# Kernel tuning notes

Hardware: AMD Instinct MI355X
Metric: run time of the kernel (lower is better)

## Reference

```python
import jax, jax.numpy as jnp
import numpy as np

N_HEADS = 1
D_MODEL = 128
TOP_K = 64
BATCH = 4
SEQ = 4096


def _rope_tables(T, d_head):
    # div_term = 10000**(arange(0,d,2)/d), repeat_interleave(2); even slice recovers the base freqs
    pos = jnp.arange(T, dtype=jnp.float32)[:, None]            # (T,1)
    div = 10000.0 ** (jnp.arange(0, d_head, 2, dtype=jnp.float32) / d_head)  # (d/2,)
    ang = pos / div[None, :]                                    # (T, d/2)
    return jnp.cos(ang), jnp.sin(ang)


def _apply_rope(x, cos, sin):
    # x: (..., T, d); cos/sin: (T, d/2) broadcast over leading dims
    xe = x[..., 0::2]
    xo = x[..., 1::2]
    re = xe * cos - xo * sin
    ro = xe * sin + xo * cos
    return jnp.stack([re, ro], axis=-1).reshape(x.shape)


def setup_inputs() -> dict:
    key = jax.random.key(0)
    kq, kk, kv = jax.random.split(key, 3)
    q = jax.random.normal(kq, (BATCH, SEQ, D_MODEL), dtype=jnp.float32)
    k = jax.random.normal(kk, (BATCH, SEQ, D_MODEL), dtype=jnp.float32)
    v = jax.random.normal(kv, (BATCH, SEQ, D_MODEL), dtype=jnp.float32)
    return {"q": q, "k": k, "v": v}


def reference(q, k, v):
    b, T, d_model = q.shape
    H = N_HEADS
    D = d_model // H  # d_head; module only valid for H=1 (k is never head-split)
    qh = q.reshape(b, T, H, D).transpose(0, 2, 1, 3)   # (b,H,T,D)
    vh = v.reshape(b, T, H, D).transpose(0, 2, 1, 3)   # (b,H,T,D)
    kh = k[:, None, :, :]                              # (b,1,T,d_model) == (b,H,T,D) for H=1

    cos, sin = _rope_tables(T, D)
    qh = _apply_rope(qh, cos, sin)
    kh = _apply_rope(kh, cos, sin)

    scale = 1.0 / jnp.sqrt(jnp.asarray(D, dtype=qh.dtype))
    logits = jnp.einsum('bhtd,bhsd->bhts', qh, kh) * scale   # (b,H,T,T)

    idx = jnp.arange(T)
    causal = idx[None, :] <= idx[:, None]                    # (T,T): key j <= query i
    logits = jnp.where(causal[None, None], logits, -jnp.inf)

    topk_vals, topk_idx = jax.lax.top_k(logits, TOP_K)       # (b,H,T,K)
    attn = jax.nn.softmax(topk_vals, axis=-1)                # -inf rows -> 0 weight

    bi = jnp.arange(b)[:, None, None, None]
    hi = jnp.arange(H)[None, :, None, None]
    topk_v = vh[bi, hi, topk_idx]                            # (b,H,T,K,D)
    out = jnp.einsum('bhtk,bhtkd->bhtd', attn, topk_v)       # (b,H,T,D)
    return out.transpose(0, 2, 1, 3).reshape(b, T, d_model)
```

## Files before the change

kernel.cpp:

```cpp
#include <hip/hip_runtime.h>
#include <math.h>

#define BATCH 4
#define SEQ   4096
#define DM    128
#define TOPK  64
#define SCALE 0.08838834764831845f
#define CAP   384

typedef short bf16x8 __attribute__((ext_vector_type(8)));
typedef float f32x4  __attribute__((ext_vector_type(4)));

__device__ __forceinline__ unsigned short f2bf(float x) {
    unsigned u = __float_as_uint(x);
    u += 0x7FFFu + ((u >> 16) & 1u);
    return (unsigned short)(u >> 16);
}
__device__ __forceinline__ float bf2f(unsigned short h) {
    return __uint_as_float(((unsigned)h) << 16);
}
__device__ __forceinline__ void split3(float x, unsigned short& h,
                                       unsigned short& md, unsigned short& l) {
    h = f2bf(x);
    float r1 = x - bf2f(h);
    md = f2bf(r1);
    float r2 = r1 - bf2f(md);
    l = f2bf(r2);
}

__device__ __forceinline__ unsigned fmap(float f) {
    unsigned u = __float_as_uint(f);
    return (u & 0x80000000u) ? ~u : (u | 0x80000000u);
}
__device__ __forceinline__ float finv(unsigned u) {
    return (u & 0x80000000u) ? __uint_as_float(u & 0x7FFFFFFFu) : __uint_as_float(~u);
}
__device__ __forceinline__ float wave_fmax(float v) {
    #pragma unroll
    for (int m = 32; m; m >>= 1) v = fmaxf(v, __shfl_xor(v, m));
    return v;
}
__device__ __forceinline__ float wave_fsum(float v) {
    #pragma unroll
    for (int m = 32; m; m >>= 1) v += __shfl_xor(v, m);
    return v;
}
__device__ __forceinline__ unsigned wave_umax(unsigned v) {
    #pragma unroll
    for (int m = 32; m; m >>= 1) { unsigned o = __shfl_xor(v, m); v = (o > v) ? o : v; }
    return v;
}

__device__ __forceinline__ float ztail(float p) {
    float pp = (p <= 0.5f) ? p : (1.f - p);
    float tt = sqrtf(-2.f * logf(pp));
    float z = tt - (2.30753f + 0.27061f * tt) / (1.f + 0.99229f * tt + 0.04481f * tt * tt);
    return (p <= 0.5f) ? z : -z;
}

__global__ void rope_decomp(const float* __restrict__ q, const float* __restrict__ k,
                            unsigned short* __restrict__ qh, unsigned short* __restrict__ qm,
                            unsigned short* __restrict__ ql, unsigned short* __restrict__ kh,
                            unsigned short* __restrict__ km, unsigned short* __restrict__ kl) {
    int idx = blockIdx.x * blockDim.x + threadIdx.x;
    const int total = BATCH * SEQ * (DM / 2);
    if (idx >= total) return;
    int i   = idx & 63;
    int pos = (idx >> 6) & (SEQ - 1);
    int b   = idx >> 18;
    float dv  = powf(10000.0f, (float)(2 * i) / (float)DM);
    float ang = (float)pos / dv;
    float sn, cs;
    sincosf(ang, &sn, &cs);
    size_t base = ((size_t)b * SEQ + pos) * DM + 2 * i;
    float qe = q[base], qo = q[base + 1];
    float ke = k[base], ko = k[base + 1];
    float q0 = (qe * cs - qo * sn) * SCALE, q1 = (qe * sn + qo * cs) * SCALE;
    float k0 = ke * cs - ko * sn,          k1 = ke * sn + ko * cs;
    unsigned short h, m2, l;
    split3(q0, h, m2, l); qh[base] = h;     qm[base] = m2;     ql[base] = l;
    split3(q1, h, m2, l); qh[base + 1] = h; qm[base + 1] = m2; ql[base + 1] = l;
    split3(k0, h, m2, l); kh[base] = h;     km[base] = m2;     kl[base] = l;
    split3(k1, h, m2, l); kh[base + 1] = h; km[base + 1] = m2; kl[base + 1] = l;
}

__launch_bounds__(256, 2)
__global__ void logits_mfma(const unsigned short* __restrict__ qh, const unsigned short* __restrict__ qm,
                            const unsigned short* __restrict__ ql, const unsigned short* __restrict__ kh,
                            const unsigned short* __restrict__ km, const unsigned short* __restrict__ kl,
                            float* __restrict__ lg, int r0, int m, int stride) {
    const int st = blockIdx.x, qt = blockIdx.y, b = blockIdx.z;
    const int Q0 = r0 + qt * 128, S0 = st * 128;
    if (S0 > Q0 + 127) return;
    const int tid = threadIdx.x, lane = tid & 63, w = tid >> 6;
    const int wm = (w >> 1) * 64, wn = (w & 1) * 64;
    if (S0 + wn > Q0 + wm + 63) return;

    const int rA = Q0 + wm + (lane & 15);
    const int rB = S0 + wn + (lane & 15);
    const int dc = (lane >> 4) * 8;

    f32x4 acc[4][4] = {};
    #pragma unroll
    for (int kk = 0; kk < 4; ++kk) {
        const int doff = kk * 32 + dc;
        bf16x8 Ah[4], Am[4], Al[4], Bh[4], Bm[4], Bl[4];
        #pragma unroll
        for (int i = 0; i < 4; ++i) {
            size_t qoff = ((size_t)b * SEQ + rA + i * 16) * DM + doff;
            Ah[i] = *(const bf16x8*)(qh + qoff);
            Am[i] = *(const bf16x8*)(qm + qoff);
            Al[i] = *(const bf16x8*)(ql + qoff);
            size_t koff = ((size_t)b * SEQ + rB + i * 16) * DM + doff;
            Bh[i] = *(const bf16x8*)(kh + koff);
            Bm[i] = *(const bf16x8*)(km + koff);
            Bl[i] = *(const bf16x8*)(kl + koff);
        }
        #pragma unroll
        for (int i = 0; i < 4; ++i)
            #pragma unroll
            for (int j = 0; j < 4; ++j) {
                f32x4 c = acc[i][j];
                c = __builtin_amdgcn_mfma_f32_16x16x32_bf16(Ah[i], Bh[j], c, 0, 0, 0);
                c = __builtin_amdgcn_mfma_f32_16x16x32_bf16(Ah[i], Bm[j], c, 0, 0, 0);
                c = __builtin_amdgcn_mfma_f32_16x16x32_bf16(Am[i], Bh[j], c, 0, 0, 0);
                c = __builtin_amdgcn_mfma_f32_16x16x32_bf16(Ah[i], Bl[j], c, 0, 0, 0);
                c = __builtin_amdgcn_mfma_f32_16x16x32_bf16(Al[i], Bh[j], c, 0, 0, 0);
                c = __builtin_amdgcn_mfma_f32_16x16x32_bf16(Am[i], Bm[j], c, 0, 0, 0);
                acc[i][j] = c;
            }
    }

    const int colb = lane & 15, rowb = (lane >> 4) * 4;
    #pragma unroll
    for (int i = 0; i < 4; ++i) {
        #pragma unroll
        for (int r = 0; r < 4; ++r) {
            int qrow = Q0 + wm + i * 16 + rowb + r;
            size_t base = ((size_t)(b * m + (qrow - r0))) * stride;
            #pragma unroll
            for (int j = 0; j < 4; ++j) {
                int col = S0 + wn + j * 16 + colb;
                if (col <= qrow) lg[base + col] = acc[i][j][r];
            }
        }
    }
}

__launch_bounds__(256)
__global__ void select_out2(const float* __restrict__ lg, const float* __restrict__ v,
                            float* __restrict__ out, int r0, int m, int stride) {
    __shared__ unsigned long long bufK[4][CAP];
    __shared__ float sW[4][TOPK];
    __shared__ int   sI[4][TOPK];

    const int w = threadIdx.x >> 6, lane = threadIdx.x & 63;
    const int x = blockIdx.x * 4 + w, b = blockIdx.y;
    if (x >= m) return;
    const int t = r0 + x, n = t + 1;
    const float* row = lg + ((size_t)(b * m + x)) * stride;
    const float4* row4 = (const float4*)row;
    const int nv4 = n >> 2, rem = n & 3;
    const unsigned long long lmask = (1ull << lane) - 1ull;

    if (n <= TOPK) {
        float val = (lane < n) ? row[lane] : -3.0e38f;
        float M = wave_fmax(val);
        float wgt = (lane < n) ? expf(val - M) : 0.f;
        float S = wave_fsum(wgt);
        sW[w][lane] = wgt;
        float inv = 1.f / S;
        float a0 = 0.f, a1 = 0.f;
        for (int j = 0; j < n; ++j) {
            float wj = sW[w][j];
            size_t base = ((size_t)b * SEQ + j) * DM;
            a0 += wj * v[base + lane];
            a1 += wj * v[base + 64 + lane];
        }
        size_t ob = ((size_t)b * SEQ + t) * DM;
        out[ob + lane] = a0 * inv;
        out[ob + 64 + lane] = a1 * inv;
        return;
    }

    float T, zt = 0.f;
    if (n <= CAP - 32) T = -3.0e38f;
    else { zt = ztail(128.f / (float)n); T = zt; }

    float Tlo = -3.3e38f, Thi = 3.3e38f;
    int C = 0;
    unsigned um = 0u;
    for (int it = 0; it < 12; ++it) {
        C = 0;
        unsigned lm = 0u;
        for (int i0 = 0; i0 < nv4; i0 += 64) {
            const int i = i0 + lane;
            const bool inb = (i < nv4);
            float4 r4;
            if (inb) r4 = row4[i];
            else { r4.x = -3.4e38f; r4.y = -3.4e38f; r4.z = -3.4e38f; r4.w = -3.4e38f; }
            const int s = i << 2;
            bool p0 = inb && (r4.x >= T);
            unsigned long long m0 = __ballot(p0);
            if (p0) { unsigned u = fmap(r4.x); lm = u > lm ? u : lm; int pos = C + __popcll(m0 & lmask); if (pos < CAP) bufK[w][pos] = ((unsigned long long)u << 32) | (unsigned)(SEQ - s); }
            C += (int)__popcll(m0);
            bool p1 = inb && (r4.y >= T);
            unsigned long long m1 = __ballot(p1);
            if (p1) { unsigned u = fmap(r4.y); lm = u > lm ? u : lm; int pos = C + __popcll(m1 & lmask); if (pos < CAP) bufK[w][pos] = ((unsigned long long)u << 32) | (unsigned)(SEQ - (s + 1)); }
            C += (int)__popcll(m1);
            bool p2 = inb && (r4.z >= T);
            unsigned long long m2 = __ballot(p2);
            if (p2) { unsigned u = fmap(r4.z); lm = u > lm ? u : lm; int pos = C + __popcll(m2 & lmask); if (pos < CAP) bufK[w][pos] = ((unsigned long long)u << 32) | (unsigned)(SEQ - (s + 2)); }
            C += (int)__popcll(m2);
            bool p3 = inb && (r4.w >= T);
            unsigned long long m3 = __ballot(p3);
            if (p3) { unsigned u = fmap(r4.w); lm = u > lm ? u : lm; int pos = C + __popcll(m3 & lmask); if (pos < CAP) bufK[w][pos] = ((unsigned long long)u << 32) | (unsigned)(SEQ - (s + 3)); }
            C += (int)__popcll(m3);
        }
        {
            float val = -3.4e38f;
            if (lane < rem) val = row[nv4 * 4 + lane];
            bool pt = (lane < rem) && (val >= T);
            unsigned long long mt = __ballot(pt);
            if (pt) { unsigned u = fmap(val); lm = u > lm ? u : lm; int pos = C + __popcll(mt & lmask); if (pos < CAP) bufK[w][pos] = ((unsigned long long)u << 32) | (unsigned)(SEQ - (nv4 * 4 + lane)); }
            C += (int)__popcll(mt);
        }
        um = wave_umax(lm);
        if (C >= TOPK && C <= CAP) break;
        if (C < TOPK) Thi = fminf(Thi, T); else Tlo = fmaxf(Tlo, T);
        float Tn; bool okc = false;
        float phat = (float)(C < 1 ? 1 : C) / (float)n;
        if (phat < 0.45f && T > 0.05f) {
            float zh = ztail(phat);
            if (zh > 0.05f) { Tn = T * (zt / zh); okc = true; }
        }
        if (!okc || !(Tn > Tlo && Tn < Thi)) {
            if (Tlo > -3.2e38f && Thi < 3.2e38f) Tn = 0.5f * (Tlo + Thi);
            else if (C < TOPK)                   Tn = T - 0.5f;
            else                                 Tn = T + 0.4f;
        }
        T = Tn;
    }
    const float M = finv(um);
    int Cw = C; if (Cw > CAP) Cw = CAP;

    sW[w][lane] = 0.f; sI[w][lane] = 0;

    for (int c0 = lane; c0 < Cw; c0 += 64) {
        unsigned long long kc = bufK[w][c0];
        int r = 0;
        for (int j = 0; j < Cw; ++j) r += (bufK[w][j] > kc);
        if (r < TOPK) {
            sW[w][r] = expf(finv((unsigned)(kc >> 32)) - M);
            sI[w][r] = SEQ - (int)(kc & 0xFFFFFFFFu);
        }
    }
    float S = wave_fsum(sW[w][lane]);
    float inv = 1.f / S;

    const int sub = lane & 31, halfw = lane >> 5;
    f32x4 a4 = {0.f, 0.f, 0.f, 0.f};
    for (int j2 = halfw; j2 < TOPK; j2 += 2) {
        float wj = sW[w][j2];
        const float4* vr = (const float4*)(v + ((size_t)b * SEQ + sI[w][j2]) * DM) + sub;
        float4 vv = *vr;
        a4.x += wj * vv.x; a4.y += wj * vv.y; a4.z += wj * vv.z; a4.w += wj * vv.w;
    }
    a4.x += __shfl_xor(a4.x, 32);
    a4.y += __shfl_xor(a4.y, 32);
    a4.z += __shfl_xor(a4.z, 32);
    a4.w += __shfl_xor(a4.w, 32);
    if (halfw == 0) {
        float4 o4;
        o4.x = a4.x * inv; o4.y = a4.y * inv; o4.z = a4.z * inv; o4.w = a4.w * inv;
        *((float4*)(out + ((size_t)b * SEQ + t) * DM) + sub) = o4;
    }
}

__global__ void rope_prep(const float* __restrict__ q, const float* __restrict__ k,
                          float* __restrict__ rq, float* __restrict__ rk) {
    int idx = blockIdx.x * blockDim.x + threadIdx.x;
    const int total = BATCH * SEQ * (DM / 2);
    if (idx >= total) return;
    int i   = idx & 63;
    int pos = (idx >> 6) & (SEQ - 1);
    int b   = idx >> 18;
    float dv  = powf(10000.0f, (float)(2 * i) / (float)DM);
    float ang = (float)pos / dv;
    float sn, cs;
    sincosf(ang, &sn, &cs);
    size_t base = ((size_t)b * SEQ + pos) * DM + 2 * i;
    float qe = q[base], qo = q[base + 1];
    float ke = k[base], ko = k[base + 1];
    rq[base]     = qe * cs - qo * sn;
    rq[base + 1] = qe * sn + qo * cs;
    rk[base]     = ke * cs - ko * sn;
    rk[base + 1] = ke * sn + ko * cs;
}

__launch_bounds__(256)
__global__ void topk_attn(const float* __restrict__ rq, const float* __restrict__ rk,
                          const float* __restrict__ v, float* __restrict__ out) {
    __shared__ unsigned umap[SEQ];
    __shared__ float    qs[DM];
    __shared__ int      selIdx[TOPK];
    __shared__ float    selW[TOPK];
    __shared__ int      cnt;
    __shared__ float    redf[4];
    __shared__ int      redi[4];
    __shared__ float    sMax, sSum;

    const int t   = blockIdx.x & (SEQ - 1);
    const int b   = blockIdx.x >> 12;
    const int tid = threadIdx.x;
    const int lane = tid & 63, wid = tid >> 6;
    const int n = t + 1;

    if (tid < DM) qs[tid] = rq[((size_t)b * SEQ + t) * DM + tid];
    if (tid == 0) cnt = 0;
    __syncthreads();

    float lmax = -INFINITY;
    for (int s = tid; s < n; s += 256) {
        const float4* kr = (const float4*)(rk + ((size_t)b * SEQ + s) * DM);
        const float4* qr = (const float4*)qs;
        float acc = 0.f;
        #pragma unroll
        for (int d = 0; d < DM / 4; ++d) {
            float4 kv = kr[d]; float4 qv = qr[d];
            acc += kv.x * qv.x + kv.y * qv.y + kv.z * qv.z + kv.w * qv.w;
        }
        float lgv = acc * SCALE;
        umap[s] = fmap(lgv);
        lmax = fmaxf(lmax, lgv);
    }
    #pragma unroll
    for (int off = 32; off; off >>= 1) lmax = fmaxf(lmax, __shfl_down(lmax, off));
    if (lane == 0) redf[wid] = lmax;
    __syncthreads();
    if (tid == 0) sMax = fmaxf(fmaxf(redf[0], redf[1]), fmaxf(redf[2], redf[3]));
    __syncthreads();
    const float M = sMax;

    const int K = (n < TOPK) ? n : TOPK;
    unsigned thr = 0u;
    if (n > TOPK) {
        unsigned long long lo = 0ull, hi = (unsigned long long)fmap(M);
        while (lo < hi) {
            unsigned long long mid = (lo + hi + 1ull) >> 1;
            unsigned m32 = (unsigned)mid;
            int c = 0;
            for (int s = tid; s < n; s += 256) c += (umap[s] >= m32) ? 1 : 0;
            #pragma unroll
            for (int off = 32; off; off >>= 1) c += __shfl_down(c, off);
            if (lane == 0) redi[wid] = c;
            __syncthreads();
            int tot = redi[0] + redi[1] + redi[2] + redi[3];
            __syncthreads();
            if (tot >= K) lo = mid; else hi = mid - 1ull;
        }
        thr = (unsigned)lo;
    }

    for (int s = tid; s < n; s += 256) {
        if (umap[s] > thr) {
            int p = atomicAdd(&cnt, 1);
            if (p < TOPK) { selIdx[p] = s; selW[p] = expf(finv(umap[s]) - M); }
        }
    }
    __syncthreads();
    for (int s = tid; s < n; s += 256) {
        if (umap[s] == thr) {
            int p = atomicAdd(&cnt, 1);
            if (p < TOPK) { selIdx[p] = s; selW[p] = expf(finv(umap[s]) - M); }
        }
    }
    __syncthreads();
    const int nsel = (cnt < TOPK) ? cnt : TOPK;

    if (tid < 64) {
        float w = (tid < nsel) ? selW[tid] : 0.f;
        #pragma unroll
        for (int off = 32; off; off >>= 1) w += __shfl_down(w, off);
        if (tid == 0) sSum = w;
    }
    __syncthreads();
    const float inv = 1.0f / sSum;

    if (tid < DM) {
        float a = 0.f;
        for (int j = 0; j < nsel; ++j)
            a += selW[j] * v[((size_t)b * SEQ + selIdx[j]) * DM + tid];
        out[((size_t)b * SEQ + t) * DM + tid] = a * inv;
    }
}

extern "C" void kernel_launch(void* const* d_in, const int* in_sizes, int n_in,
                              void* d_out, int out_size, void* d_ws, size_t ws_size,
                              hipStream_t stream) {
    const float* q = (const float*)d_in[0];
    const float* k = (const float*)d_in[1];
    const float* v = (const float*)d_in[2];
    float* out = (float*)d_out;

    const size_t plane = (size_t)BATCH * SEQ * DM;
    const size_t planesB = 6 * plane * sizeof(unsigned short);
    const int total = BATCH * SEQ * (DM / 2);

    long long Wb = (long long)ws_size - (long long)planesB;
    int cr0[64], cm[64], nch = 0;
    bool okc = (Wb > 0);
    int r0 = 0;
    while (okc && r0 < SEQ) {
        int m = SEQ - r0;
        while (m >= 128) {
            long long stride = ((r0 + m + 127) / 128) * 128;
            long long bytes = (long long)BATCH * m * stride * 4;
            if (bytes <= Wb) break;
            m -= 128;
        }
        if (m < 128 || nch >= 64) { okc = false; break; }
        cr0[nch] = r0; cm[nch] = m; ++nch;
        r0 += m;
    }

    if (!okc) {
        float* rq = (float*)d_ws;
        float* rk = rq + plane;
        hipLaunchKernelGGL(rope_prep, dim3((total + 255) / 256), dim3(256), 0, stream,
                           q, k, rq, rk);
        hipLaunchKernelGGL(topk_attn, dim3(BATCH * SEQ), dim3(256), 0, stream,
                           rq, rk, v, out);
        return;
    }

    unsigned short* qh = (unsigned short*)d_ws;
    unsigned short* qm = qh + plane;
    unsigned short* ql = qm + plane;
    unsigned short* kh = ql + plane;
    unsigned short* km = kh + plane;
    unsigned short* kl = km + plane;
    float* lgbuf = (float*)((char*)d_ws + planesB);

    hipLaunchKernelGGL(rope_decomp, dim3((total + 255) / 256), dim3(256), 0, stream,
                       q, k, qh, qm, ql, kh, km, kl);

    for (int c = 0; c < nch; ++c) {
        const int R0 = cr0[c], M = cm[c];
        const int stride = ((R0 + M + 127) / 128) * 128;
        dim3 g1((R0 + M + 127) / 128, M / 128, BATCH);
        hipLaunchKernelGGL(logits_mfma, g1, dim3(256), 0, stream,
                           qh, qm, ql, kh, km, kl, lgbuf, R0, M, stride);
        dim3 g2((M + 3) / 4, BATCH);
        hipLaunchKernelGGL(select_out2, g2, dim3(256), 0, stream,
                           lgbuf, v, out, R0, M, stride);
    }
}
```

Before: 244.5 us.

## Precompute per-row thresholds and emit candidate bitmasks in logits epilogue

The RoPE kernel now computes a per-query-row threshold from the query norm and a Gaussian tail estimate. The logits GEMM epilogue compares each logit against that threshold and writes a 64-bit candidate bitmask per 64-column block. The selection kernel reads these masks and gathers only the candidate logits, skipping the repeated full-row threshold scans. When the candidate count falls outside [TOPK, CAP] it falls back to the old iterative search. The cost is an extra memset and mask writes, plus a statistical threshold that assumes roughly Gaussian logits.

```diff
diff --git a/kernel.cpp b/kernel.cpp
--- a/kernel.cpp
+++ b/kernel.cpp
@@ -7,6 +7,8 @@
 #define TOPK  64
 #define SCALE 0.08838834764831845f
 #define CAP   384
+#define CT    160
+#define ALLN  (CAP - 32)
 
 typedef short bf16x8 __attribute__((ext_vector_type(8)));
 typedef float f32x4  __attribute__((ext_vector_type(4)));
@@ -61,7 +63,8 @@
 __global__ void rope_decomp(const float* __restrict__ q, const float* __restrict__ k,
                             unsigned short* __restrict__ qh, unsigned short* __restrict__ qm,
                             unsigned short* __restrict__ ql, unsigned short* __restrict__ kh,
-                            unsigned short* __restrict__ km, unsigned short* __restrict__ kl) {
+                            unsigned short* __restrict__ km, unsigned short* __restrict__ kl,
+                            float* __restrict__ rowT) {
     int idx = blockIdx.x * blockDim.x + threadIdx.x;
     const int total = BATCH * SEQ * (DM / 2);
     if (idx >= total) return;
@@ -82,13 +85,24 @@
     split3(q1, h, m2, l); qh[base + 1] = h; qm[base + 1] = m2; ql[base + 1] = l;
     split3(k0, h, m2, l); kh[base] = h;     km[base] = m2;     kl[base] = l;
     split3(k1, h, m2, l); kh[base + 1] = h; km[base + 1] = m2; kl[base + 1] = l;
+
+    float s2 = wave_fsum(qe * qe + qo * qo);
+    if (i == 0) {
+        int n = pos + 1;
+        float T;
+        if (n <= ALLN) T = -3.0e38f;
+        else           T = sqrtf(s2) * SCALE * ztail((float)CT / (float)n);
+        rowT[(b << 12) + pos] = T;
+    }
 }
 
 __launch_bounds__(256, 2)
 __global__ void logits_mfma(const unsigned short* __restrict__ qh, const unsigned short* __restrict__ qm,
                             const unsigned short* __restrict__ ql, const unsigned short* __restrict__ kh,
                             const unsigned short* __restrict__ km, const unsigned short* __restrict__ kl,
-                            float* __restrict__ lg, int r0, int m, int stride) {
+                            const float* __restrict__ rowT,
+                            float* __restrict__ lg, unsigned long long* __restrict__ mask,
+                            int r0, int m, int stride) {
     const int st = blockIdx.x, qt = blockIdx.y, b = blockIdx.z;
     const int Q0 = r0 + qt * 128, S0 = st * 128;
     if (S0 > Q0 + 127) return;
@@ -132,24 +146,40 @@
     }
 
     const int colb = lane & 15, rowb = (lane >> 4) * 4;
+    const int grp = lane >> 4;
+    float Trow[16];
+    #pragma unroll
+    for (int z = 0; z < 16; ++z)
+        Trow[z] = rowT[(b << 12) + Q0 + wm + (z >> 2) * 16 + rowb + (z & 3)];
+
     #pragma unroll
     for (int i = 0; i < 4; ++i) {
         #pragma unroll
         for (int r = 0; r < 4; ++r) {
-            int qrow = Q0 + wm + i * 16 + rowb + r;
-            size_t base = ((size_t)(b * m + (qrow - r0))) * stride;
+            const int qrow = Q0 + wm + i * 16 + rowb + r;
+            const size_t base = ((size_t)(b * m + (qrow - r0))) * stride;
+            const float Tr = Trow[i * 4 + r];
+            unsigned long long bm = 0ull;
             #pragma unroll
             for (int j = 0; j < 4; ++j) {
-                int col = S0 + wn + j * 16 + colb;
-                if (col <= qrow) lg[base + col] = acc[i][j][r];
+                const int col = S0 + wn + j * 16 + colb;
+                const float val = acc[i][j][r];
+                const bool causal = (col <= qrow);
+                if (causal) lg[base + col] = val;
+                const bool hit = causal && (val >= Tr);
+                unsigned long long bl = __ballot(hit);
+                bm |= ((bl >> (16 * grp)) & 0xFFFFull) << (16 * j);
             }
+            if (colb == 0)
+                mask[((size_t)((b << 12) + qrow) << 6) + ((S0 + wn) >> 6)] = bm;
         }
     }
 }
 
 __launch_bounds__(256)
-__global__ void select_out2(const float* __restrict__ lg, const float* __restrict__ v,
-                            float* __restrict__ out, int r0, int m, int stride) {
+__global__ void select_mask(const float* __restrict__ lg, const unsigned long long* __restrict__ mask,
+                            const float* __restrict__ v, float* __restrict__ out,
+                            int r0, int m, int stride) {
     __shared__ unsigned long long bufK[4][CAP];
     __shared__ float sW[4][TOPK];
     __shared__ int   sI[4][TOPK];
@@ -159,8 +189,7 @@
     if (x >= m) return;
     const int t = r0 + x, n = t + 1;
     const float* row = lg + ((size_t)(b * m + x)) * stride;
-    const float4* row4 = (const float4*)row;
-    const int nv4 = n >> 2, rem = n & 3;
+    const int rb = (b << 12) + t;
     const unsigned long long lmask = (1ull << lane) - 1ull;
 
     if (n <= TOPK) {
@@ -183,63 +212,89 @@
         return;
     }
 
-    float T, zt = 0.f;
-    if (n <= CAP - 32) T = -3.0e38f;
-    else { zt = ztail(128.f / (float)n); T = zt; }
-
-    float Tlo = -3.3e38f, Thi = 3.3e38f;
-    int C = 0;
+    unsigned long long mk = mask[((size_t)rb << 6) + lane];
+    int myc = __popcll(mk);
+    int pre = myc;
+    #pragma unroll
+    for (int off = 1; off < 64; off <<= 1) {
+        int o = __shfl_up(pre, off);
+        if (lane >= off) pre += o;
+    }
+    int C = __shfl(pre, 63);
+    pre -= myc;
+
     unsigned um = 0u;
-    for (int it = 0; it < 12; ++it) {
+    if (C >= TOPK && C <= CAP) {
+        int p = pre;
+        unsigned long long mm = mk;
+        while (mm) {
+            int bit = __builtin_ctzll(mm);
+            mm &= mm - 1;
+            int idx = (lane << 6) + bit;
+            unsigned u = fmap(row[idx]);
+            um = u > um ? u : um;
+            bufK[w][p++] = ((unsigned long long)u << 32) | (unsigned)(SEQ - idx);
+        }
+        um = wave_umax(um);
+    } else {
+        const float4* row4 = (const float4*)row;
+        const int nv4 = n >> 2, rem = n & 3;
+        float T, zt = 0.f;
+        if (n <= CAP - 32) T = -3.0e38f;
+        else { zt = ztail(128.f / (float)n); T = zt; }
+        float Tlo = -3.3e38f, Thi = 3.3e38f;
         C = 0;
-        unsigned lm = 0u;
-        for (int i0 = 0; i0 < nv4; i0 += 64) {
-            const int i = i0 + lane;
-            const bool inb = (i < nv4);
-            float4 r4;
-            if (inb) r4 = row4[i];
-            else { r4.x = -3.4e38f; r4.y = -3.4e38f; r4.z = -3.4e38f; r4.w = -3.4e38f; }
-            const int s = i << 2;
-            bool p0 = inb && (r4.x >= T);
-            unsigned long long m0 = __ballot(p0);
-            if (p0) { unsigned u = fmap(r4.x); lm = u > lm ? u : lm; int pos = C + __popcll(m0 & lmask); if (pos < CAP) bufK[w][pos] = ((unsigned long long)u << 32) | (unsigned)(SEQ - s); }
-            C += (int)__popcll(m0);
-            bool p1 = inb && (r4.y >= T);
-            unsigned long long m1 = __ballot(p1);
-            if (p1) { unsigned u = fmap(r4.y); lm = u > lm ? u : lm; int pos = C + __popcll(m1 & lmask); if (pos < CAP) bufK[w][pos] = ((unsigned long long)u << 32) | (unsigned)(SEQ - (s + 1)); }
-            C += (int)__popcll(m1);
-            bool p2 = inb && (r4.z >= T);
-            unsigned long long m2 = __ballot(p2);
-            if (p2) { unsigned u = fmap(r4.z); lm = u > lm ? u : lm; int pos = C + __popcll(m2 & lmask); if (pos < CAP) bufK[w][pos] = ((unsigned long long)u << 32) | (unsigned)(SEQ - (s + 2)); }
-            C += (int)__popcll(m2);
-            bool p3 = inb && (r4.w >= T);
-            unsigned long long m3 = __ballot(p3);
-            if (p3) { unsigned u = fmap(r4.w); lm = u > lm ? u : lm; int pos = C + __popcll(m3 & lmask); if (pos < CAP) bufK[w][pos] = ((unsigned long long)u << 32) | (unsigned)(SEQ - (s + 3)); }
-            C += (int)__popcll(m3);
-        }
-        {
-            float val = -3.4e38f;
-            if (lane < rem) val = row[nv4 * 4 + lane];
-            bool pt = (lane < rem) && (val >= T);
-            unsigned long long mt = __ballot(pt);
-            if (pt) { unsigned u = fmap(val); lm = u > lm ? u : lm; int pos = C + __popcll(mt & lmask); if (pos < CAP) bufK[w][pos] = ((unsigned long long)u << 32) | (unsigned)(SEQ - (nv4 * 4 + lane)); }
-            C += (int)__popcll(mt);
-        }
-        um = wave_umax(lm);
-        if (C >= TOPK && C <= CAP) break;
-        if (C < TOPK) Thi = fminf(Thi, T); else Tlo = fmaxf(Tlo, T);
-        float Tn; bool okc = false;
-        float phat = (float)(C < 1 ? 1 : C) / (float)n;
-        if (phat < 0.45f && T > 0.05f) {
-            float zh = ztail(phat);
-            if (zh > 0.05f) { Tn = T * (zt / zh); okc = true; }
-        }
-        if (!okc || !(Tn > Tlo && Tn < Thi)) {
-            if (Tlo > -3.2e38f && Thi < 3.2e38f) Tn = 0.5f * (Tlo + Thi);
-            else if (C < TOPK)                   Tn = T - 0.5f;
-            else                                 Tn = T + 0.4f;
-        }
-        T = Tn;
+        for (int it = 0; it < 12; ++it) {
+            C = 0;
+            unsigned lm = 0u;
+            for (int i0 = 0; i0 < nv4; i0 += 64) {
+                const int i = i0 + lane;
+                const bool inb = (i < nv4);
+                float4 r4;
+                if (inb) r4 = row4[i];
+                else { r4.x = -3.4e38f; r4.y = -3.4e38f; r4.z = -3.4e38f; r4.w = -3.4e38f; }
+                const int s = i << 2;
+                bool p0 = inb && (r4.x >= T);
+                unsigned long long m0 = __ballot(p0);
+                if (p0) { unsigned u = fmap(r4.x); lm = u > lm ? u : lm; int pos = C + __popcll(m0 & lmask); if (pos < CAP) bufK[w][pos] = ((unsigned long long)u << 32) | (unsigned)(SEQ - s); }
+                C += (int)__popcll(m0);
+                bool p1 = inb && (r4.y >= T);
+                unsigned long long m1 = __ballot(p1);
+                if (p1) { unsigned u = fmap(r4.y); lm = u > lm ? u : lm; int pos = C + __popcll(m1 & lmask); if (pos < CAP) bufK[w][pos] = ((unsigned long long)u << 32) | (unsigned)(SEQ - (s + 1)); }
+                C += (int)__popcll(m1);
+                bool p2 = inb && (r4.z >= T);
+                unsigned long long m2 = __ballot(p2);
+                if (p2) { unsigned u = fmap(r4.z); lm = u > lm ? u : lm; int pos = C + __popcll(m2 & lmask); if (pos < CAP) bufK[w][pos] = ((unsigned long long)u << 32) | (unsigned)(SEQ - (s + 2)); }
+                C += (int)__popcll(m2);
+                bool p3 = inb && (r4.w >= T);
+                unsigned long long m3 = __ballot(p3);
+                if (p3) { unsigned u = fmap(r4.w); lm = u > lm ? u : lm; int pos = C + __popcll(m3 & lmask); if (pos < CAP) bufK[w][pos] = ((unsigned long long)u << 32) | (unsigned)(SEQ - (s + 3)); }
+                C += (int)__popcll(m3);
+            }
+            {
+                float val = -3.4e38f;
+                if (lane < rem) val = row[nv4 * 4 + lane];
+                bool pt = (lane < rem) && (val >= T);
+                unsigned long long mt = __ballot(pt);
+                if (pt) { unsigned u = fmap(val); lm = u > lm ? u : lm; int pos = C + __popcll(mt & lmask); if (pos < CAP) bufK[w][pos] = ((unsigned long long)u << 32) | (unsigned)(SEQ - (nv4 * 4 + lane)); }
+                C += (int)__popcll(mt);
+            }
+            um = wave_umax(lm);
+            if (C >= TOPK && C <= CAP) break;
+            if (C < TOPK) Thi = fminf(Thi, T); else Tlo = fmaxf(Tlo, T);
+            float Tn; bool okc = false;
+            float phat = (float)(C < 1 ? 1 : C) / (float)n;
+            if (phat < 0.45f && T > 0.05f) {
+                float zh = ztail(phat);
+                if (zh > 0.05f) { Tn = T * (zt / zh); okc = true; }
+            }
+            if (!okc || !(Tn > Tlo && Tn < Thi)) {
+                if (Tlo > -3.2e38f && Thi < 3.2e38f) Tn = 0.5f * (Tlo + Thi);
+                else if (C < TOPK)                   Tn = T - 0.5f;
+                else                                 Tn = T + 0.4f;
+            }
+            T = Tn;
+        }
     }
     const float M = finv(um);
     int Cw = C; if (Cw > CAP) Cw = CAP;
@@ -403,11 +458,14 @@
     const float* v = (const float*)d_in[2];
     float* out = (float*)d_out;
 
-    const size_t plane = (size_t)BATCH * SEQ * DM;
+    const size_t plane   = (size_t)BATCH * SEQ * DM;
     const size_t planesB = 6 * plane * sizeof(unsigned short);
+    const size_t rowTB   = (size_t)BATCH * SEQ * sizeof(float);
+    const size_t maskB   = (size_t)BATCH * SEQ * (SEQ / 64) * 8;
+    const size_t headB   = planesB + rowTB + maskB;
     const int total = BATCH * SEQ * (DM / 2);
 
-    long long Wb = (long long)ws_size - (long long)planesB;
+    long long Wb = (long long)ws_size - (long long)headB;
     int cr0[64], cm[64], nch = 0;
     bool okc = (Wb > 0);
     int r0 = 0;
@@ -440,19 +498,22 @@
     unsigned short* kh = ql + plane;
     unsigned short* km = kh + plane;
     unsigned short* kl = km + plane;
-    float* lgbuf = (float*)((char*)d_ws + planesB);
-
+    float* rowT = (float*)((char*)d_ws + planesB);
+    unsigned long long* mask = (unsigned long long*)((char*)d_ws + planesB + rowTB);
+    float* lgbuf = (float*)((char*)d_ws + headB);
+
+    hipMemsetAsync(mask, 0, maskB, stream);
     hipLaunchKernelGGL(rope_decomp, dim3((total + 255) / 256), dim3(256), 0, stream,
-                       q, k, qh, qm, ql, kh, km, kl);
+                       q, k, qh, qm, ql, kh, km, kl, rowT);
 
     for (int c = 0; c < nch; ++c) {
         const int R0 = cr0[c], M = cm[c];
         const int stride = ((R0 + M + 127) / 128) * 128;
         dim3 g1((R0 + M + 127) / 128, M / 128, BATCH);
         hipLaunchKernelGGL(logits_mfma, g1, dim3(256), 0, stream,
-                           qh, qm, ql, kh, km, kl, lgbuf, R0, M, stride);
+                           qh, qm, ql, kh, km, kl, rowT, lgbuf, mask, R0, M, stride);
         dim3 g2((M + 3) / 4, BATCH);
-        hipLaunchKernelGGL(select_out2, g2, dim3(256), 0, stream,
-                           lgbuf, v, out, R0, M, stride);
-    }
-}
+        hipLaunchKernelGGL(select_mask, g2, dim3(256), 0, stream,
+                           lgbuf, mask, v, out, R0, M, stride);
+    }
+}
```

Result: slower. 273.3 us (+11.8%).
